# Performance work log

Measured on AMD Instinct MI355X. Metric: run time of the kernel, lower is better.

Reference implementation:

```python
import jax, jax.numpy as jnp
import numpy as np

N = 100000
D = 64
H = 4 * D  # 256
E = 1000000


def setup_inputs() -> dict:
    key = jax.random.key(0)
    ks = jax.random.split(key, 9)
    return {
        "loc_feat": jax.random.normal(ks[0], (N, D), dtype=jnp.float32),
        "geo_src": jax.random.randint(ks[1], (E,), 0, N),
        "geo_dst": jax.random.randint(ks[2], (E,), 0, N),
        "trans_src": jax.random.randint(ks[3], (E,), 0, N),
        "trans_dst": jax.random.randint(ks[4], (E,), 0, N),
        "trans_w": jax.random.uniform(ks[5], (E,), dtype=jnp.float32),
        "W1": jax.random.normal(ks[6], (D, H), dtype=jnp.float32) * (1.0 / np.sqrt(D)),
        "b1": jax.random.normal(ks[7], (H,), dtype=jnp.float32) * 0.01,
        "W2": jax.random.normal(ks[8], (H, 1), dtype=jnp.float32) * (1.0 / np.sqrt(H)),
    }


def reference(loc_feat, geo_src, geo_dst, trans_src, trans_dst, trans_w, W1, b1, W2):
    n = loc_feat.shape[0]
    # etype 'geo': copy_u + mean  -> segment mean of src features at dst
    geo_sum = jax.ops.segment_sum(loc_feat[geo_src], geo_dst, num_segments=n)
    cnt = jax.ops.segment_sum(jnp.ones(geo_src.shape[0], loc_feat.dtype), geo_dst, num_segments=n)
    geo = jnp.where(cnt[:, None] > 0, geo_sum / jnp.maximum(cnt, 1.0)[:, None], 0.0)
    # etype 'trans': u_mul_e + sum -> weighted segment sum
    trans = jax.ops.segment_sum(loc_feat[trans_src] * trans_w[:, None], trans_dst, num_segments=n)
    # semantic attention fuse over the two relation views
    z = jnp.stack([geo, trans], axis=1)          # [N, 2, D]
    h = jnp.tanh(jnp.einsum('nkd,dh->nkh', z, W1) + b1)  # [N, 2, H]
    w = jnp.einsum('nkh,ho->nko', h, W2).mean(0)  # [2, 1] (mean over nodes)
    beta = jax.nn.softmax(w, axis=0)              # [2, 1]
    return (beta[None, :, :] * z).sum(1)          # [N, D]
```

## Files before the change

kernel.cpp:

```cpp
#include <hip/hip_runtime.h>
#include <hip/hip_bf16.h>

#define N_NODES 100000
#define DIM 64
#define HID 256
#define E_EDGES 1000000
#define TWO_N (2 * N_NODES)
#define MLP_ROWBLOCKS (TWO_N / 64)

#define TILE 60
#define NBINS 1667
#define CAP 800
#define EPB 4096
#define FILL_BLOCKS 245

typedef short short8 __attribute__((ext_vector_type(8)));
typedef float f32x4 __attribute__((ext_vector_type(4)));
typedef unsigned short us4 __attribute__((ext_vector_type(4)));
typedef unsigned short us8 __attribute__((ext_vector_type(8)));

__device__ __forceinline__ float tanh_fast(float x) {
    x = fminf(fmaxf(x, -15.0f), 15.0f);
    float e = __expf(2.0f * x);
    return (e - 1.0f) / (e + 1.0f);
}

__device__ __forceinline__ unsigned short f2bf(float x) {
    unsigned u = __float_as_uint(x);
    u = u + 0x7FFFu + ((u >> 16) & 1u);
    return (unsigned short)(u >> 16);
}

__device__ __forceinline__ float bf2f(unsigned short u) {
    return __uint_as_float(((unsigned)u) << 16);
}

__global__ void pack_feat_kernel(const float* __restrict__ feat,
                                 unsigned short* __restrict__ fb) {
    int i = blockIdx.x * 256 + threadIdx.x;
    float4 v = ((const float4*)feat)[i];
    us4 o;
    o[0] = f2bf(v.x); o[1] = f2bf(v.y); o[2] = f2bf(v.z); o[3] = f2bf(v.w);
    ((us4*)fb)[i] = o;
}

__global__ void __launch_bounds__(512) bin_fill_kernel(
        const int* __restrict__ gs, const int* __restrict__ gd,
        const int* __restrict__ ts, const int* __restrict__ td,
        const float* __restrict__ tw,
        int* __restrict__ gcount,
        int* __restrict__ gbin, int2* __restrict__ tbin) {
    __shared__ int   hist[NBINS];
    __shared__ int   adjS[NBINS];
    __shared__ int   curS[NBINS];
    __shared__ int   pS[EPB];
    __shared__ float w2S[EPB];
    __shared__ unsigned short binS[EPB];
    __shared__ int   wsumS[8];
    __shared__ int   wpreS[8];

    int t = threadIdx.x;
    int lane = t & 63, wv = t >> 6;
    int blk = blockIdx.x;
    int rel = (blk >= FILL_BLOCKS) ? 1 : 0;
    int e0 = (rel ? blk - FILL_BLOCKS : blk) * EPB;
    const int* dstp = rel ? td : gd;
    const int* srcp = rel ? ts : gs;

    for (int i = t; i < NBINS; i += 512) hist[i] = 0;
    __syncthreads();

    int d_[8], s_[8];
    float w_[8];
    #pragma unroll
    for (int j = 0; j < 2; ++j) {
        int idx = e0 + j * 2048 + 4 * t;
        if (idx + 3 < E_EDGES) {
            int4 dv = *(const int4*)&dstp[idx];
            int4 sv = *(const int4*)&srcp[idx];
            d_[4*j+0] = dv.x; d_[4*j+1] = dv.y; d_[4*j+2] = dv.z; d_[4*j+3] = dv.w;
            s_[4*j+0] = sv.x; s_[4*j+1] = sv.y; s_[4*j+2] = sv.z; s_[4*j+3] = sv.w;
            if (rel) {
                float4 wvv = *(const float4*)&tw[idx];
                w_[4*j+0] = wvv.x; w_[4*j+1] = wvv.y; w_[4*j+2] = wvv.z; w_[4*j+3] = wvv.w;
            }
        } else {
            #pragma unroll
            for (int i2 = 0; i2 < 4; ++i2) {
                bool ok = (idx + i2 < E_EDGES);
                d_[4*j+i2] = ok ? dstp[idx + i2] : -1;
                s_[4*j+i2] = ok ? srcp[idx + i2] : 0;
                w_[4*j+i2] = (ok && rel) ? tw[idx + i2] : 0.0f;
            }
        }
    }
    #pragma unroll
    for (int i = 0; i < 8; ++i)
        if (d_[i] >= 0) atomicAdd(&hist[d_[i] / TILE], 1);
    __syncthreads();

    int carry = 0;
    for (int cb = 0; cb < NBINS; cb += 512) {
        int i = cb + t;
        int c = (i < NBINS) ? hist[i] : 0;
        int v = c;
        #pragma unroll
        for (int off = 1; off < 64; off <<= 1) {
            int u = __shfl_up(v, off);
            if (lane >= off) v += u;
        }
        if (lane == 63) wsumS[wv] = v;
        __syncthreads();
        if (t == 0) {
            int s = 0;
            #pragma unroll
            for (int w = 0; w < 8; ++w) { s += wsumS[w]; wpreS[w] = s; }
        }
        __syncthreads();
        int woff = (wv == 0) ? 0 : wpreS[wv - 1];
        if (i < NBINS) {
            int lb = carry + woff + v - c;
            curS[i] = lb;
            int gb = (c > 0) ? (i * CAP + atomicAdd(&gcount[rel * NBINS + i], c)) : 0;
            adjS[i] = gb - lb;
        }
        carry += wpreS[7];
        __syncthreads();
    }
    __syncthreads();

    #pragma unroll
    for (int i = 0; i < 8; ++i) {
        int d = d_[i];
        if (d < 0) continue;
        int bin = d / TILE;
        int pos = atomicAdd(&curS[bin], 1);
        pS[pos] = s_[i] | ((d - bin * TILE) << 20);
        binS[pos] = (unsigned short)bin;
        if (rel) w2S[pos] = w_[i];
    }
    __syncthreads();

    int nV = min(EPB, E_EDGES - e0);
    if (!rel) {
        for (int i = t; i < nV; i += 512) {
            int b = binS[i];
            int gi = adjS[b] + i;
            if (gi < (b + 1) * CAP)
                gbin[gi] = pS[i];
        }
    } else {
        for (int i = t; i < nV; i += 512) {
            int b = binS[i];
            int gi = adjS[b] + i;
            if (gi < (b + 1) * CAP)
                tbin[gi] = make_int2(pS[i], __float_as_int(w2S[i]));
        }
    }
}

__global__ void __launch_bounds__(256) aggregate_kernel(
        const unsigned short* __restrict__ featb,
        const int* __restrict__ gbin, const int2* __restrict__ tbin,
        const int* __restrict__ gcount,
        unsigned short* __restrict__ zb) {
    __shared__ int   srcS[CAP];
    __shared__ float wS[CAP];
    __shared__ int   histS[TILE];
    __shared__ int   baseS[TILE];
    __shared__ int   curS[TILE];

    int b = blockIdx.x;
    int rel = (b >= NBINS) ? 1 : 0;
    int bin = rel ? b - NBINS : b;
    int node0 = bin * TILE;
    int nNodes = min(TILE, N_NODES - node0);
    int t = threadIdx.x, lane = t & 63, wave = t >> 6;
    int oct = lane >> 3;
    int co = (lane & 7) * 8;

    int nE = gcount[b];
    if (nE > CAP) nE = CAP;

    for (int i = t; i < TILE; i += 256) histS[i] = 0;
    __syncthreads();

    if (!rel) {
        const int* bp = gbin + (size_t)bin * CAP;
        for (int i = t; i < nE; i += 256) atomicAdd(&histS[bp[i] >> 20], 1);
    } else {
        const int2* bp = tbin + (size_t)bin * CAP;
        for (int i = t; i < nE; i += 256) atomicAdd(&histS[bp[i].x >> 20], 1);
    }
    __syncthreads();

    if (t < 64) {
        int c = (t < TILE) ? histS[t] : 0;
        int v = c;
        #pragma unroll
        for (int off = 1; off < 64; off <<= 1) {
            int u = __shfl_up(v, off);
            if (t >= off) v += u;
        }
        if (t < TILE) {
            int b0 = v - c;
            baseS[t] = b0;
            curS[t] = b0;
        }
    }
    __syncthreads();

    if (!rel) {
        const int* bp = gbin + (size_t)bin * CAP;
        for (int i = t; i < nE; i += 256) {
            int p = bp[i];
            int pos = atomicAdd(&curS[p >> 20], 1);
            srcS[pos] = p & 0xFFFFF;
        }
    } else {
        const int2* bp = tbin + (size_t)bin * CAP;
        for (int i = t; i < nE; i += 256) {
            int2 p = bp[i];
            int pos = atomicAdd(&curS[p.x >> 20], 1);
            srcS[pos] = p.x & 0xFFFFF;
            wS[pos] = __int_as_float(p.y);
        }
    }
    __syncthreads();

    for (int nl0 = wave * 8; nl0 < nNodes; nl0 += 32) {
        int nl = nl0 + oct;
        bool act = (nl < nNodes);
        int deg = act ? histS[nl] : 0;
        int base = act ? baseS[nl] : 0;
        float a[8] = {0.f, 0.f, 0.f, 0.f, 0.f, 0.f, 0.f, 0.f};
        if (!rel) {
            int k = 0;
            for (; k + 3 < deg; k += 4) {
                int s0 = srcS[base + k],     s1 = srcS[base + k + 1];
                int s2 = srcS[base + k + 2], s3 = srcS[base + k + 3];
                us8 r0 = *(const us8*)&featb[(size_t)s0 * DIM + co];
                us8 r1 = *(const us8*)&featb[(size_t)s1 * DIM + co];
                us8 r2 = *(const us8*)&featb[(size_t)s2 * DIM + co];
                us8 r3 = *(const us8*)&featb[(size_t)s3 * DIM + co];
                #pragma unroll
                for (int j = 0; j < 8; ++j)
                    a[j] += (bf2f(r0[j]) + bf2f(r1[j])) + (bf2f(r2[j]) + bf2f(r3[j]));
            }
            for (; k < deg; ++k) {
                int s = srcS[base + k];
                us8 r = *(const us8*)&featb[(size_t)s * DIM + co];
                #pragma unroll
                for (int j = 0; j < 8; ++j) a[j] += bf2f(r[j]);
            }
        } else {
            int k = 0;
            for (; k + 3 < deg; k += 4) {
                int s0 = srcS[base + k],     s1 = srcS[base + k + 1];
                int s2 = srcS[base + k + 2], s3 = srcS[base + k + 3];
                float w0 = wS[base + k],     w1 = wS[base + k + 1];
                float w2 = wS[base + k + 2], w3 = wS[base + k + 3];
                us8 r0 = *(const us8*)&featb[(size_t)s0 * DIM + co];
                us8 r1 = *(const us8*)&featb[(size_t)s1 * DIM + co];
                us8 r2 = *(const us8*)&featb[(size_t)s2 * DIM + co];
                us8 r3 = *(const us8*)&featb[(size_t)s3 * DIM + co];
                #pragma unroll
                for (int j = 0; j < 8; ++j)
                    a[j] += (bf2f(r0[j]) * w0 + bf2f(r1[j]) * w1)
                          + (bf2f(r2[j]) * w2 + bf2f(r3[j]) * w3);
            }
            for (; k < deg; ++k) {
                int s = srcS[base + k];
                float w = wS[base + k];
                us8 r = *(const us8*)&featb[(size_t)s * DIM + co];
                #pragma unroll
                for (int j = 0; j < 8; ++j) a[j] += bf2f(r[j]) * w;
            }
        }
        if (act) {
            float sc = rel ? 1.0f : 1.0f / fmaxf((float)deg, 1.0f);
            us8 o;
            #pragma unroll
            for (int j = 0; j < 8; ++j) o[j] = f2bf(a[j] * sc);
            size_t row = (size_t)(rel ? N_NODES + node0 + nl : node0 + nl);
            *(us8*)&zb[row * DIM + co] = o;
        }
    }
}

__global__ void pack_w1_kernel(const float* __restrict__ W1, unsigned short* __restrict__ W1p) {
    int i = blockIdx.x * 256 + threadIdx.x;
    int j = i & 7;
    int r = i >> 3;
    int nidx = r & 15; r >>= 4;
    int q = r & 3; r >>= 2;
    int khalf = r & 1;
    int n = r >> 1;
    int k = 32 * khalf + 8 * q + j;
    int c = 16 * n + nidx;
    W1p[i] = f2bf(W1[k * HID + c]);
}

__global__ void __launch_bounds__(256) mlp_mfma_kernel(
        const unsigned short* __restrict__ zb,
        const unsigned short* __restrict__ W1p,
        const float* __restrict__ bias1, const float* __restrict__ W2,
        float* __restrict__ partials) {
    __shared__ float wred[4][2];
    int t = threadIdx.x, lane = t & 63, wave = t >> 6;
    int m = lane & 15, q = lane >> 4;
    int base = blockIdx.x * 64 + wave * 16;
    int R = base + m;

    const unsigned short* rowp = zb + (size_t)R * DIM;
    short8 a0 = *(const short8*)(rowp + q * 8);
    short8 a1 = *(const short8*)(rowp + 32 + q * 8);

    float c0 = 0.0f, c1 = 0.0f;
    const short8* W1v = (const short8*)W1p;

    #pragma unroll 4
    for (int n = 0; n < 16; ++n) {
        short8 b0 = W1v[(n * 2 + 0) * 64 + lane];
        short8 bK = W1v[(n * 2 + 1) * 64 + lane];
        f32x4 acc = {0.0f, 0.0f, 0.0f, 0.0f};
        acc = __builtin_amdgcn_mfma_f32_16x16x32_bf16(a0, b0, acc, 0, 0, 0);
        acc = __builtin_amdgcn_mfma_f32_16x16x32_bf16(a1, bK, acc, 0, 0, 0);
        int col = 16 * n + m;
        float bj = bias1[col];
        float w2 = W2[col];
        #pragma unroll
        for (int reg = 0; reg < 4; ++reg) {
            int Rr = base + q * 4 + reg;
            float h = tanh_fast(acc[reg] + bj);
            float contrib = h * w2;
            if (Rr < N_NODES) c0 += contrib; else c1 += contrib;
        }
    }

    #pragma unroll
    for (int off = 32; off > 0; off >>= 1) {
        c0 += __shfl_down(c0, off);
        c1 += __shfl_down(c1, off);
    }
    if (lane == 0) { wred[wave][0] = c0; wred[wave][1] = c1; }
    __syncthreads();
    if (t == 0) {
        partials[blockIdx.x * 2 + 0] = wred[0][0] + wred[1][0] + wred[2][0] + wred[3][0];
        partials[blockIdx.x * 2 + 1] = wred[0][1] + wred[1][1] + wred[2][1] + wred[3][1];
    }
}

__global__ void beta_kernel(const float* __restrict__ partials, float* __restrict__ beta) {
    __shared__ float wred[4][2];
    int t = threadIdx.x;
    float c0 = 0.0f, c1 = 0.0f;
    for (int i = t; i < MLP_ROWBLOCKS; i += 256) {
        c0 += partials[i * 2 + 0];
        c1 += partials[i * 2 + 1];
    }
    #pragma unroll
    for (int off = 32; off > 0; off >>= 1) {
        c0 += __shfl_down(c0, off);
        c1 += __shfl_down(c1, off);
    }
    int lane = t & 63, wv = t >> 6;
    if (lane == 0) { wred[wv][0] = c0; wred[wv][1] = c1; }
    __syncthreads();
    if (t == 0) {
        float s0 = (wred[0][0] + wred[1][0] + wred[2][0] + wred[3][0]) / (float)N_NODES;
        float s1 = (wred[0][1] + wred[1][1] + wred[2][1] + wred[3][1]) / (float)N_NODES;
        float m = fmaxf(s0, s1);
        float e0 = __expf(s0 - m), e1 = __expf(s1 - m);
        float inv = 1.0f / (e0 + e1);
        beta[0] = e0 * inv;
        beta[1] = e1 * inv;
    }
}

__global__ void combine_kernel(const unsigned short* __restrict__ zb,
                               const float* __restrict__ beta,
                               float* __restrict__ out) {
    int gid = blockIdx.x * 256 + threadIdx.x;
    float b0 = beta[0];
    float b1 = beta[1];
    uint4 g = *(const uint4*)&zb[(size_t)gid * 8];
    uint4 tr = *(const uint4*)&zb[(size_t)N_NODES * DIM + (size_t)gid * 8];
    float4 o0, o1;
    o0.x = b0 * __uint_as_float(g.x << 16) + b1 * __uint_as_float(tr.x << 16);
    o0.y = b0 * __uint_as_float(g.x & 0xFFFF0000u) + b1 * __uint_as_float(tr.x & 0xFFFF0000u);
    o0.z = b0 * __uint_as_float(g.y << 16) + b1 * __uint_as_float(tr.y << 16);
    o0.w = b0 * __uint_as_float(g.y & 0xFFFF0000u) + b1 * __uint_as_float(tr.y & 0xFFFF0000u);
    o1.x = b0 * __uint_as_float(g.z << 16) + b1 * __uint_as_float(tr.z << 16);
    o1.y = b0 * __uint_as_float(g.z & 0xFFFF0000u) + b1 * __uint_as_float(tr.z & 0xFFFF0000u);
    o1.z = b0 * __uint_as_float(g.w << 16) + b1 * __uint_as_float(tr.w << 16);
    o1.w = b0 * __uint_as_float(g.w & 0xFFFF0000u) + b1 * __uint_as_float(tr.w & 0xFFFF0000u);
    *(float4*)&out[(size_t)gid * 8] = o0;
    *(float4*)&out[(size_t)gid * 8 + 4] = o1;
}

extern "C" void kernel_launch(void* const* d_in, const int* in_sizes, int n_in,
                              void* d_out, int out_size, void* d_ws, size_t ws_size,
                              hipStream_t stream) {
    const float* loc_feat = (const float*)d_in[0];
    const int* geo_src    = (const int*)d_in[1];
    const int* geo_dst    = (const int*)d_in[2];
    const int* trans_src  = (const int*)d_in[3];
    const int* trans_dst  = (const int*)d_in[4];
    const float* trans_w  = (const float*)d_in[5];
    const float* W1       = (const float*)d_in[6];
    const float* b1       = (const float*)d_in[7];
    const float* W2       = (const float*)d_in[8];
    float* out = (float*)d_out;

    int*   gcount   = (int*)d_ws;
    int*   gbin     = gcount + 2 * NBINS;
    int2*  tbin     = (int2*)(gbin + (size_t)NBINS * CAP);
    float* partials = (float*)(tbin + (size_t)NBINS * CAP);
    float* beta     = partials + 2 * MLP_ROWBLOCKS;
    unsigned short* W1p   = (unsigned short*)(beta + 2);
    unsigned short* featb = W1p + 16384;
    unsigned short* zb    = featb + (size_t)N_NODES * DIM;

    hipMemsetAsync(gcount, 0, 2 * NBINS * sizeof(int), stream);

    pack_feat_kernel<<<(N_NODES * DIM / 4) / 256, 256, 0, stream>>>(loc_feat, featb);
    pack_w1_kernel<<<64, 256, 0, stream>>>(W1, W1p);
    bin_fill_kernel<<<2 * FILL_BLOCKS, 512, 0, stream>>>(geo_src, geo_dst, trans_src,
                                                         trans_dst, trans_w,
                                                         gcount, gbin, tbin);
    aggregate_kernel<<<2 * NBINS, 256, 0, stream>>>(featb, gbin, tbin, gcount, zb);
    mlp_mfma_kernel<<<MLP_ROWBLOCKS, 256, 0, stream>>>(zb, W1p, b1, W2, partials);
    beta_kernel<<<1, 256, 0, stream>>>(partials, beta);
    combine_kernel<<<(N_NODES * DIM / 8) / 256, 256, 0, stream>>>(zb, beta, out);
}
```

Baseline: 236.8 us.

## Fuse prep kernels, fold beta into combine, sub-sort edges by source chunk

Packing of features and W1 now runs inside the edge-binning kernel as extra blocks, which saves two launches and lets the three jobs run concurrently. The beta softmax reduction is folded into every combine block, so each block recomputes the same small reduction over the partials instead of paying for a separate launch. In the aggregate kernel, edges within each destination node are also ordered by source-index chunk (8 chunks) using a multi-wave scan, so that gathers from feature memory have better locality. The cost is a longer scan with more syncs, and redundant partial reductions spread across all combine blocks.

After: 238.0 us. Within noise of the previous version (+0.5%).

```diff
diff --git a/kernel.cpp b/kernel.cpp
--- a/kernel.cpp
+++ b/kernel.cpp
@@ -14,6 +14,13 @@
 #define EPB 4096
 #define FILL_BLOCKS 245
 
+#define NCH 8
+#define KEYS (TILE * NCH)
+
+#define PACKF_BLOCKS 782
+#define PACKW1_BLOCKS 32
+#define PREP_BLOCKS (2 * FILL_BLOCKS + PACKF_BLOCKS + PACKW1_BLOCKS)
+
 typedef short short8 __attribute__((ext_vector_type(8)));
 typedef float f32x4 __attribute__((ext_vector_type(4)));
 typedef unsigned short us4 __attribute__((ext_vector_type(4)));
@@ -35,21 +42,14 @@
     return __uint_as_float(((unsigned)u) << 16);
 }
 
-__global__ void pack_feat_kernel(const float* __restrict__ feat,
-                                 unsigned short* __restrict__ fb) {
-    int i = blockIdx.x * 256 + threadIdx.x;
-    float4 v = ((const float4*)feat)[i];
-    us4 o;
-    o[0] = f2bf(v.x); o[1] = f2bf(v.y); o[2] = f2bf(v.z); o[3] = f2bf(v.w);
-    ((us4*)fb)[i] = o;
-}
-
-__global__ void __launch_bounds__(512) bin_fill_kernel(
+__global__ void __launch_bounds__(512) prep_kernel(
         const int* __restrict__ gs, const int* __restrict__ gd,
         const int* __restrict__ ts, const int* __restrict__ td,
         const float* __restrict__ tw,
         int* __restrict__ gcount,
-        int* __restrict__ gbin, int2* __restrict__ tbin) {
+        int* __restrict__ gbin, int2* __restrict__ tbin,
+        const float* __restrict__ feat, unsigned short* __restrict__ fb,
+        const float* __restrict__ W1, unsigned short* __restrict__ W1p) {
     __shared__ int   hist[NBINS];
     __shared__ int   adjS[NBINS];
     __shared__ int   curS[NBINS];
@@ -60,8 +60,37 @@
     __shared__ int   wpreS[8];
 
     int t = threadIdx.x;
+    int blk = blockIdx.x;
+
+    if (blk >= 2 * FILL_BLOCKS) {
+        int pb = blk - 2 * FILL_BLOCKS;
+        if (pb < PACKF_BLOCKS) {
+            #pragma unroll
+            for (int j = 0; j < 4; ++j) {
+                int i = pb * 2048 + j * 512 + t;
+                if (i < N_NODES * DIM / 4) {
+                    float4 v = ((const float4*)feat)[i];
+                    us4 o;
+                    o[0] = f2bf(v.x); o[1] = f2bf(v.y); o[2] = f2bf(v.z); o[3] = f2bf(v.w);
+                    ((us4*)fb)[i] = o;
+                }
+            }
+        } else {
+            int i = (pb - PACKF_BLOCKS) * 512 + t;
+            int j = i & 7;
+            int r = i >> 3;
+            int nidx = r & 15; r >>= 4;
+            int q = r & 3; r >>= 2;
+            int khalf = r & 1;
+            int n = r >> 1;
+            int k = 32 * khalf + 8 * q + j;
+            int c = 16 * n + nidx;
+            W1p[i] = f2bf(W1[k * HID + c]);
+        }
+        return;
+    }
+
     int lane = t & 63, wv = t >> 6;
-    int blk = blockIdx.x;
     int rel = (blk >= FILL_BLOCKS) ? 1 : 0;
     int e0 = (rel ? blk - FILL_BLOCKS : blk) * EPB;
     const int* dstp = rel ? td : gd;
@@ -166,9 +195,13 @@
         unsigned short* __restrict__ zb) {
     __shared__ int   srcS[CAP];
     __shared__ float wS[CAP];
-    __shared__ int   histS[TILE];
-    __shared__ int   baseS[TILE];
-    __shared__ int   curS[TILE];
+    __shared__ int   histK[KEYS];
+    __shared__ int   keyBase[KEYS];
+    __shared__ int   keyCur[KEYS];
+    __shared__ int   nodeB[TILE];
+    __shared__ int   nodeD[TILE];
+    __shared__ int   wsA[4];
+    __shared__ int   wpA[4];
 
     int b = blockIdx.x;
     int rel = (b >= NBINS) ? 1 : 0;
@@ -182,31 +215,58 @@
     int nE = gcount[b];
     if (nE > CAP) nE = CAP;
 
-    for (int i = t; i < TILE; i += 256) histS[i] = 0;
+    for (int i = t; i < KEYS; i += 256) histK[i] = 0;
     __syncthreads();
 
     if (!rel) {
         const int* bp = gbin + (size_t)bin * CAP;
-        for (int i = t; i < nE; i += 256) atomicAdd(&histS[bp[i] >> 20], 1);
+        for (int i = t; i < nE; i += 256) {
+            int p = bp[i];
+            int key = ((p >> 20) << 3) | ((p & 0xFFFFF) >> 14);
+            atomicAdd(&histK[key], 1);
+        }
     } else {
         const int2* bp = tbin + (size_t)bin * CAP;
-        for (int i = t; i < nE; i += 256) atomicAdd(&histS[bp[i].x >> 20], 1);
-    }
-    __syncthreads();
-
-    if (t < 64) {
-        int c = (t < TILE) ? histS[t] : 0;
+        for (int i = t; i < nE; i += 256) {
+            int p = bp[i].x;
+            int key = ((p >> 20) << 3) | ((p & 0xFFFFF) >> 14);
+            atomicAdd(&histK[key], 1);
+        }
+    }
+    __syncthreads();
+
+    int carry = 0;
+    for (int cb = 0; cb < KEYS; cb += 256) {
+        int i = cb + t;
+        int c = (i < KEYS) ? histK[i] : 0;
         int v = c;
         #pragma unroll
         for (int off = 1; off < 64; off <<= 1) {
             int u = __shfl_up(v, off);
-            if (t >= off) v += u;
-        }
-        if (t < TILE) {
-            int b0 = v - c;
-            baseS[t] = b0;
-            curS[t] = b0;
-        }
+            if (lane >= off) v += u;
+        }
+        if (lane == 63) wsA[wave] = v;
+        __syncthreads();
+        if (t == 0) {
+            int s = 0;
+            #pragma unroll
+            for (int w = 0; w < 4; ++w) { s += wsA[w]; wpA[w] = s; }
+        }
+        __syncthreads();
+        int woff = (wave == 0) ? 0 : wpA[wave - 1];
+        if (i < KEYS) {
+            int lb = carry + woff + v - c;
+            keyBase[i] = lb;
+            keyCur[i] = lb;
+        }
+        carry += wpA[3];
+        __syncthreads();
+    }
+    if (t < TILE) {
+        int nb = keyBase[t * NCH];
+        int nx = (t == TILE - 1) ? nE : keyBase[(t + 1) * NCH];
+        nodeB[t] = nb;
+        nodeD[t] = nx - nb;
     }
     __syncthreads();
 
@@ -214,14 +274,16 @@
         const int* bp = gbin + (size_t)bin * CAP;
         for (int i = t; i < nE; i += 256) {
             int p = bp[i];
-            int pos = atomicAdd(&curS[p >> 20], 1);
+            int key = ((p >> 20) << 3) | ((p & 0xFFFFF) >> 14);
+            int pos = atomicAdd(&keyCur[key], 1);
             srcS[pos] = p & 0xFFFFF;
         }
     } else {
         const int2* bp = tbin + (size_t)bin * CAP;
         for (int i = t; i < nE; i += 256) {
             int2 p = bp[i];
-            int pos = atomicAdd(&curS[p.x >> 20], 1);
+            int key = ((p.x >> 20) << 3) | ((p.x & 0xFFFFF) >> 14);
+            int pos = atomicAdd(&keyCur[key], 1);
             srcS[pos] = p.x & 0xFFFFF;
             wS[pos] = __int_as_float(p.y);
         }
@@ -231,8 +293,8 @@
     for (int nl0 = wave * 8; nl0 < nNodes; nl0 += 32) {
         int nl = nl0 + oct;
         bool act = (nl < nNodes);
-        int deg = act ? histS[nl] : 0;
-        int base = act ? baseS[nl] : 0;
+        int deg = act ? nodeD[nl] : 0;
+        int base = act ? nodeB[nl] : 0;
         float a[8] = {0.f, 0.f, 0.f, 0.f, 0.f, 0.f, 0.f, 0.f};
         if (!rel) {
             int k = 0;
@@ -286,19 +348,6 @@
             *(us8*)&zb[row * DIM + co] = o;
         }
     }
-}
-
-__global__ void pack_w1_kernel(const float* __restrict__ W1, unsigned short* __restrict__ W1p) {
-    int i = blockIdx.x * 256 + threadIdx.x;
-    int j = i & 7;
-    int r = i >> 3;
-    int nidx = r & 15; r >>= 4;
-    int q = r & 3; r >>= 2;
-    int khalf = r & 1;
-    int n = r >> 1;
-    int k = 32 * khalf + 8 * q + j;
-    int c = 16 * n + nidx;
-    W1p[i] = f2bf(W1[k * HID + c]);
 }
 
 __global__ void __launch_bounds__(256) mlp_mfma_kernel(
@@ -351,9 +400,14 @@
     }
 }
 
-__global__ void beta_kernel(const float* __restrict__ partials, float* __restrict__ beta) {
+__global__ void __launch_bounds__(256) combine_kernel(
+        const unsigned short* __restrict__ zb,
+        const float* __restrict__ partials,
+        float* __restrict__ out) {
     __shared__ float wred[4][2];
-    int t = threadIdx.x;
+    __shared__ float bS[2];
+    int t = threadIdx.x, lane = t & 63, wv = t >> 6;
+
     float c0 = 0.0f, c1 = 0.0f;
     for (int i = t; i < MLP_ROWBLOCKS; i += 256) {
         c0 += partials[i * 2 + 0];
@@ -364,7 +418,6 @@
         c0 += __shfl_down(c0, off);
         c1 += __shfl_down(c1, off);
     }
-    int lane = t & 63, wv = t >> 6;
     if (lane == 0) { wred[wv][0] = c0; wred[wv][1] = c1; }
     __syncthreads();
     if (t == 0) {
@@ -373,17 +426,14 @@
         float m = fmaxf(s0, s1);
         float e0 = __expf(s0 - m), e1 = __expf(s1 - m);
         float inv = 1.0f / (e0 + e1);
-        beta[0] = e0 * inv;
-        beta[1] = e1 * inv;
-    }
-}
-
-__global__ void combine_kernel(const unsigned short* __restrict__ zb,
-                               const float* __restrict__ beta,
-                               float* __restrict__ out) {
-    int gid = blockIdx.x * 256 + threadIdx.x;
-    float b0 = beta[0];
-    float b1 = beta[1];
+        bS[0] = e0 * inv;
+        bS[1] = e1 * inv;
+    }
+    __syncthreads();
+    float b0 = bS[0];
+    float b1 = bS[1];
+
+    int gid = blockIdx.x * 256 + t;
     uint4 g = *(const uint4*)&zb[(size_t)gid * 8];
     uint4 tr = *(const uint4*)&zb[(size_t)N_NODES * DIM + (size_t)gid * 8];
     float4 o0, o1;
@@ -424,13 +474,11 @@
 
     hipMemsetAsync(gcount, 0, 2 * NBINS * sizeof(int), stream);
 
-    pack_feat_kernel<<<(N_NODES * DIM / 4) / 256, 256, 0, stream>>>(loc_feat, featb);
-    pack_w1_kernel<<<64, 256, 0, stream>>>(W1, W1p);
-    bin_fill_kernel<<<2 * FILL_BLOCKS, 512, 0, stream>>>(geo_src, geo_dst, trans_src,
-                                                         trans_dst, trans_w,
-                                                         gcount, gbin, tbin);
+    prep_kernel<<<PREP_BLOCKS, 512, 0, stream>>>(geo_src, geo_dst, trans_src,
+                                                 trans_dst, trans_w,
+                                                 gcount, gbin, tbin,
+                                                 loc_feat, featb, W1, W1p);
     aggregate_kernel<<<2 * NBINS, 256, 0, stream>>>(featb, gbin, tbin, gcount, zb);
     mlp_mfma_kernel<<<MLP_ROWBLOCKS, 256, 0, stream>>>(zb, W1p, b1, W2, partials);
-    beta_kernel<<<1, 256, 0, stream>>>(partials, beta);
-    combine_kernel<<<(N_NODES * DIM / 8) / 256, 256, 0, stream>>>(zb, beta, out);
-}
+    combine_kernel<<<(N_NODES * DIM / 8) / 256, 256, 0, stream>>>(zb, partials, out);
+}
```
